# Kernel optimization log

Measured on AMD Instinct MI355X. Metric: run time of the kernel, lower is better.

Reference implementation:

```python
import jax, jax.numpy as jnp
import numpy as np

DECAY = 0.2
THRESH = 0.5
LENS = 0.5  # surrogate-gradient window half-width

@jax.custom_vjp
def spike(mem):
    # Heaviside spike at threshold (standard BP-SNN act_fun)
    return (mem > THRESH).astype(mem.dtype)

def _spike_fwd(mem):
    return spike(mem), mem

def _spike_bwd(mem, g):
    # rectangular surrogate gradient
    surr = (jnp.abs(mem - THRESH) < LENS).astype(mem.dtype)
    return (g * surr,)

spike.defvjp(_spike_fwd, _spike_bwd)


def setup_inputs() -> dict:
    key = jax.random.key(0)
    k1, k2, k3 = jax.random.split(key, 3)
    B, T, N_IN, N_H2, N_CLS = 2048, 50, 620, 620, 11
    x = jax.random.normal(k1, (B, T, N_IN), dtype=jnp.float32)
    # PyTorch Linear default init: U(-1/sqrt(fan_in), 1/sqrt(fan_in))
    b1 = 1.0 / np.sqrt(N_IN)
    b2 = 1.0 / np.sqrt(N_H2)
    W1 = jax.random.uniform(k2, (N_H2, N_IN), jnp.float32, -b1, b1)
    W2 = jax.random.uniform(k3, (N_CLS, N_H2), jnp.float32, -b2, b2)
    return {"x": x, "W1": W1, "W2": W2}


def reference(x, W1, W2):
    B = x.shape[0]
    T = x.shape[1]
    n_h2 = W1.shape[0]   # 620
    n_cls = W2.shape[0]  # 11

    def step(carry, xt):
        h1_mem, h1_spk, h2_mem, h2_spk, acc = carry
        # mem_update for layer 1: fc = Linear(no bias) + ReLU
        h1_mem = h1_mem * DECAY * (1.0 - h1_spk) + jax.nn.relu(xt @ W1.T)
        h1_spk = spike(h1_mem)
        # mem_update for layer 2
        h2_mem = h2_mem * DECAY * (1.0 - h2_spk) + jax.nn.relu(h1_spk @ W2.T)
        h2_spk = spike(h2_mem)
        return (h1_mem, h1_spk, h2_mem, h2_spk, acc + h2_spk), None

    z1 = jnp.zeros((B, n_h2), x.dtype)
    z2 = jnp.zeros((B, n_cls), x.dtype)
    carry0 = (z1, z1, z2, z2, z2)
    xs = jnp.swapaxes(x, 0, 1)  # [T, B, n_in]
    (_, _, _, _, sumspike), _ = jax.lax.scan(step, carry0, xs)
    return sumspike / 50.0
```

## Files before the change

kernel.cpp:

```cpp
#include <hip/hip_runtime.h>
#include <cstdint>
#include <cstddef>

#define B_TOT 2048
#define T_TOT 50
#define NIN   620
#define NH    620
#define NCLS  11

#define KC 384

#define BM 128
#define BN 128
#define KB 32

__global__ __launch_bounds__(256, 4)
void gemm_relu_kernel(const float* __restrict__ X,
                      const float* __restrict__ W1,
                      float* __restrict__ Z,
                      int t0, int ct)
{
    __shared__ float As[KB][BM + 4];
    __shared__ float Bs[KB][BN + 4];

    const int tid = threadIdx.x;
    const int n0 = blockIdx.x * BN;
    const int m0 = blockIdx.y * BM;
    const int tx = tid & 15;
    const int ty = tid >> 4;

    size_t a_off[4];
    size_t b_off[4];
    int    s_row[4], s_kl[4], b_ok[4];
#pragma unroll
    for (int it = 0; it < 4; ++it) {
        int task = tid + it * 256;
        int row  = (task >> 2) & 127;
        int kl   = (task >> 9) * 16 + (task & 3) * 4;
        s_row[it] = row;
        s_kl[it]  = kl;
        int m  = m0 + row;
        int bb = m / ct;
        int dt = m - bb * ct;
        a_off[it] = ((size_t)bb * T_TOT + (size_t)(t0 + dt)) * (size_t)NIN + kl;
        int n = n0 + row;
        b_off[it] = (size_t)n * NIN + kl;
        b_ok[it]  = (n < NH);
    }

    float acc[8][8];
#pragma unroll
    for (int i = 0; i < 8; ++i)
#pragma unroll
        for (int j = 0; j < 8; ++j) acc[i][j] = 0.0f;

    const int zc0 = n0 + tx * 4;
    const int zc1 = n0 + 64 + tx * 4;

    for (int k0 = 0; k0 < NIN; k0 += KB) {
#pragma unroll
        for (int it = 0; it < 4; ++it) {
            int k = k0 + s_kl[it];
            float4 av = make_float4(0.f, 0.f, 0.f, 0.f);
            if (k < NIN) av = *(const float4*)(X + a_off[it] + k0);
            As[s_kl[it] + 0][s_row[it]] = av.x;
            As[s_kl[it] + 1][s_row[it]] = av.y;
            As[s_kl[it] + 2][s_row[it]] = av.z;
            As[s_kl[it] + 3][s_row[it]] = av.w;
            float4 bv = make_float4(0.f, 0.f, 0.f, 0.f);
            if (b_ok[it] && k < NIN) bv = *(const float4*)(W1 + b_off[it] + k0);
            Bs[s_kl[it] + 0][s_row[it]] = bv.x;
            Bs[s_kl[it] + 1][s_row[it]] = bv.y;
            Bs[s_kl[it] + 2][s_row[it]] = bv.z;
            Bs[s_kl[it] + 3][s_row[it]] = bv.w;
        }
        __syncthreads();

#pragma unroll 8
        for (int kk = 0; kk < KB; ++kk) {
            float a[8], b[8];
            *(float4*)&a[0] = *(const float4*)&As[kk][ty * 8];
            *(float4*)&a[4] = *(const float4*)&As[kk][ty * 8 + 4];
            *(float4*)&b[0] = *(const float4*)&Bs[kk][tx * 4];
            *(float4*)&b[4] = *(const float4*)&Bs[kk][64 + tx * 4];
#pragma unroll
            for (int i = 0; i < 8; ++i)
#pragma unroll
                for (int j = 0; j < 8; ++j)
                    acc[i][j] = fmaf(a[i], b[j], acc[i][j]);
        }
        __syncthreads();

        if (k0 + KB == KC) {
#pragma unroll
            for (int i = 0; i < 8; ++i) {
                float* zr = Z + (size_t)(m0 + ty * 8 + i) * NH;
                if (zc0 < NH)
                    *(float4*)(zr + zc0) = make_float4(acc[i][0], acc[i][1],
                                                       acc[i][2], acc[i][3]);
                if (zc1 < NH)
                    *(float4*)(zr + zc1) = make_float4(acc[i][4], acc[i][5],
                                                       acc[i][6], acc[i][7]);
            }
#pragma unroll
            for (int i = 0; i < 8; ++i)
#pragma unroll
                for (int j = 0; j < 8; ++j) acc[i][j] = 0.0f;
        }
    }

#pragma unroll
    for (int i = 0; i < 8; ++i) {
        float* zr = Z + (size_t)(m0 + ty * 8 + i) * NH;
        if (zc0 < NH) {
            float4 p = *(const float4*)(zr + zc0);
            float4 v;
            v.x = fmaxf(__fadd_rn(p.x, acc[i][0]), 0.0f);
            v.y = fmaxf(__fadd_rn(p.y, acc[i][1]), 0.0f);
            v.z = fmaxf(__fadd_rn(p.z, acc[i][2]), 0.0f);
            v.w = fmaxf(__fadd_rn(p.w, acc[i][3]), 0.0f);
            *(float4*)(zr + zc0) = v;
        }
        if (zc1 < NH) {
            float4 p = *(const float4*)(zr + zc1);
            float4 v;
            v.x = fmaxf(__fadd_rn(p.x, acc[i][4]), 0.0f);
            v.y = fmaxf(__fadd_rn(p.y, acc[i][5]), 0.0f);
            v.z = fmaxf(__fadd_rn(p.z, acc[i][6]), 0.0f);
            v.w = fmaxf(__fadd_rn(p.w, acc[i][7]), 0.0f);
            *(float4*)(zr + zc1) = v;
        }
    }
}

#define NWAVE 4
__global__ __launch_bounds__(256)
void snn_kernel(const float* __restrict__ Z,
                const float* __restrict__ W2,
                float* __restrict__ state,
                float* __restrict__ out,
                int t0, int ct)
{
    __shared__ float W2s[NCLS][NH];
    __shared__ float Ss[NWAVE][NH];

    const int tid = threadIdx.x;
    for (int i = tid; i < NCLS * NH; i += 256)
        ((float*)W2s)[i] = W2[i];
    __syncthreads();

    const int lane = tid & 63;
    const int wv   = tid >> 6;
    const int b    = blockIdx.x * NWAVE + wv;

    float* st_h1m = state;
    float* st_h1s = state + (size_t)B_TOT * NH;
    float* st_h2m = state + (size_t)2 * B_TOT * NH;
    float* st_h2s = st_h2m + (size_t)B_TOT * NCLS;
    float* st_acc = st_h2s + (size_t)B_TOT * NCLS;

    float h1m[10], h1s[10];
    float h2m = 0.f, h2s = 0.f, acc = 0.f;

    if (t0 == 0) {
#pragma unroll
        for (int i = 0; i < 10; ++i) { h1m[i] = 0.f; h1s[i] = 0.f; }
    } else {
#pragma unroll
        for (int i = 0; i < 10; ++i) {
            int k = i * 64 + lane;
            if (k < NH) {
                h1m[i] = st_h1m[(size_t)b * NH + k];
                h1s[i] = st_h1s[(size_t)b * NH + k];
            } else { h1m[i] = 0.f; h1s[i] = 0.f; }
        }
        if (lane < NCLS) {
            h2m = st_h2m[(size_t)b * NCLS + lane];
            h2s = st_h2s[(size_t)b * NCLS + lane];
            acc = st_acc[(size_t)b * NCLS + lane];
        }
    }

    const int cls   = lane & 31;
    const int qbase = (lane < 32) ? 0 : (KC / 4);
    const int qcnt  = (lane < 32) ? (KC / 4) : ((NH - KC) / 4);

    for (int dt = 0; dt < ct; ++dt) {
        const float* z = Z + ((size_t)b * ct + dt) * NH;

#pragma unroll
        for (int i = 0; i < 10; ++i) {
            int k = i * 64 + lane;
            if (k < NH) {
                float dec = __fmul_rn(__fmul_rn(h1m[i], 0.2f), (1.0f - h1s[i]));
                float m = __fadd_rn(dec, z[k]);
                float s = (m > 0.5f) ? 1.0f : 0.0f;
                h1m[i] = m; h1s[i] = s;
                Ss[wv][k] = s;
            }
        }
        __syncthreads();

        float csum = 0.0f;
        if (cls < NCLS) {
            const float4* w4 = (const float4*)&W2s[cls][0] + qbase;
            const float4* s4 = (const float4*)&Ss[wv][0] + qbase;
            for (int q = 0; q < qcnt; ++q) {
                float4 w = w4[q];
                float4 s = s4[q];
                csum = fmaf(s.x, w.x, csum);
                csum = fmaf(s.y, w.y, csum);
                csum = fmaf(s.z, w.z, csum);
                csum = fmaf(s.w, w.w, csum);
            }
        }
        float csumB = __shfl_xor(csum, 32, 64);
        if (lane < NCLS) {
            float ctot = __fadd_rn(csum, csumB);
            float dec = __fmul_rn(__fmul_rn(h2m, 0.2f), (1.0f - h2s));
            float m = __fadd_rn(dec, fmaxf(ctot, 0.0f));
            float s = (m > 0.5f) ? 1.0f : 0.0f;
            h2m = m; h2s = s;
            acc = __fadd_rn(acc, s);
        }
        __syncthreads();
    }

    if (t0 + ct >= T_TOT) {
        if (lane < NCLS)
            out[(size_t)b * NCLS + lane] = __fdiv_rn(acc, 50.0f);
    } else {
#pragma unroll
        for (int i = 0; i < 10; ++i) {
            int k = i * 64 + lane;
            if (k < NH) {
                st_h1m[(size_t)b * NH + k] = h1m[i];
                st_h1s[(size_t)b * NH + k] = h1s[i];
            }
        }
        if (lane < NCLS) {
            st_h2m[(size_t)b * NCLS + lane] = h2m;
            st_h2s[(size_t)b * NCLS + lane] = h2s;
            st_acc[(size_t)b * NCLS + lane] = acc;
        }
    }
}

extern "C" void kernel_launch(void* const* d_in, const int* in_sizes, int n_in,
                              void* d_out, int out_size, void* d_ws, size_t ws_size,
                              hipStream_t stream)
{
    const float* X  = (const float*)d_in[0];
    const float* W1 = (const float*)d_in[1];
    const float* W2 = (const float*)d_in[2];
    float* out = (float*)d_out;

    const size_t state_floats = (size_t)2 * B_TOT * NH + (size_t)3 * B_TOT * NCLS;
    const size_t state_bytes  = state_floats * sizeof(float);
    const size_t bytes_per_t  = (size_t)B_TOT * NH * sizeof(float);

    size_t avail = (ws_size > state_bytes) ? (ws_size - state_bytes) : 0;
    int chunkT = (int)(avail / bytes_per_t);
    if (chunkT > T_TOT) chunkT = T_TOT;
    if (chunkT < 1) chunkT = 1;

    float* state = (float*)d_ws;
    float* Zbuf  = state + state_floats;

    for (int t0 = 0; t0 < T_TOT; t0 += chunkT) {
        int ct = (T_TOT - t0 < chunkT) ? (T_TOT - t0) : chunkT;
        dim3 ggrid((NH + BN - 1) / BN, (B_TOT * ct) / BM);
        gemm_relu_kernel<<<ggrid, 256, 0, stream>>>(X, W1, Zbuf, t0, ct);
        snn_kernel<<<dim3(B_TOT / NWAVE), 256, 0, stream>>>(Zbuf, W2, state, out, t0, ct);
    }
}
```

Before: 1.452 ms.

## Prefetch next GEMM K-tile into registers and batch LDS loads in readout dot

The layer-1 GEMM now loads the next K-tile of X and W1 into registers while the current tile is being multiplied, and stores it to shared memory after a barrier. This hides global-load latency behind the FMA loop at the cost of more registers. Separately, the layer-2 class dot-product loop is unrolled by 8, issuing batched shared-memory loads before the FMAs. The added register pressure may hurt occupancy under launch_bounds(256,4).

```diff
diff --git a/kernel.cpp b/kernel.cpp
--- a/kernel.cpp
+++ b/kernel.cpp
@@ -57,24 +57,45 @@
     const int zc0 = n0 + tx * 4;
     const int zc1 = n0 + 64 + tx * 4;
 
+    float4 pa[4], pb[4];
+
+#pragma unroll
+    for (int it = 0; it < 4; ++it) {
+        pa[it] = make_float4(0.f, 0.f, 0.f, 0.f);
+        pb[it] = make_float4(0.f, 0.f, 0.f, 0.f);
+        if (s_kl[it] < NIN) {
+            pa[it] = *(const float4*)(X + a_off[it]);
+            if (b_ok[it]) pb[it] = *(const float4*)(W1 + b_off[it]);
+        }
+    }
+#pragma unroll
+    for (int it = 0; it < 4; ++it) {
+        As[s_kl[it] + 0][s_row[it]] = pa[it].x;
+        As[s_kl[it] + 1][s_row[it]] = pa[it].y;
+        As[s_kl[it] + 2][s_row[it]] = pa[it].z;
+        As[s_kl[it] + 3][s_row[it]] = pa[it].w;
+        Bs[s_kl[it] + 0][s_row[it]] = pb[it].x;
+        Bs[s_kl[it] + 1][s_row[it]] = pb[it].y;
+        Bs[s_kl[it] + 2][s_row[it]] = pb[it].z;
+        Bs[s_kl[it] + 3][s_row[it]] = pb[it].w;
+    }
+
     for (int k0 = 0; k0 < NIN; k0 += KB) {
-#pragma unroll
-        for (int it = 0; it < 4; ++it) {
-            int k = k0 + s_kl[it];
-            float4 av = make_float4(0.f, 0.f, 0.f, 0.f);
-            if (k < NIN) av = *(const float4*)(X + a_off[it] + k0);
-            As[s_kl[it] + 0][s_row[it]] = av.x;
-            As[s_kl[it] + 1][s_row[it]] = av.y;
-            As[s_kl[it] + 2][s_row[it]] = av.z;
-            As[s_kl[it] + 3][s_row[it]] = av.w;
-            float4 bv = make_float4(0.f, 0.f, 0.f, 0.f);
-            if (b_ok[it] && k < NIN) bv = *(const float4*)(W1 + b_off[it] + k0);
-            Bs[s_kl[it] + 0][s_row[it]] = bv.x;
-            Bs[s_kl[it] + 1][s_row[it]] = bv.y;
-            Bs[s_kl[it] + 2][s_row[it]] = bv.z;
-            Bs[s_kl[it] + 3][s_row[it]] = bv.w;
-        }
         __syncthreads();
+
+        const int k0n = k0 + KB;
+        const bool has_next = (k0n < NIN);
+        if (has_next) {
+#pragma unroll
+            for (int it = 0; it < 4; ++it) {
+                pa[it] = make_float4(0.f, 0.f, 0.f, 0.f);
+                pb[it] = make_float4(0.f, 0.f, 0.f, 0.f);
+                if (k0n + s_kl[it] < NIN) {
+                    pa[it] = *(const float4*)(X + a_off[it] + k0n);
+                    if (b_ok[it]) pb[it] = *(const float4*)(W1 + b_off[it] + k0n);
+                }
+            }
+        }
 
 #pragma unroll 8
         for (int kk = 0; kk < KB; ++kk) {
@@ -89,7 +110,6 @@
                 for (int j = 0; j < 8; ++j)
                     acc[i][j] = fmaf(a[i], b[j], acc[i][j]);
         }
-        __syncthreads();
 
         if (k0 + KB == KC) {
 #pragma unroll
@@ -106,6 +126,22 @@
             for (int i = 0; i < 8; ++i)
 #pragma unroll
                 for (int j = 0; j < 8; ++j) acc[i][j] = 0.0f;
+        }
+
+        __syncthreads();
+
+        if (has_next) {
+#pragma unroll
+            for (int it = 0; it < 4; ++it) {
+                As[s_kl[it] + 0][s_row[it]] = pa[it].x;
+                As[s_kl[it] + 1][s_row[it]] = pa[it].y;
+                As[s_kl[it] + 2][s_row[it]] = pa[it].z;
+                As[s_kl[it] + 3][s_row[it]] = pa[it].w;
+                Bs[s_kl[it] + 0][s_row[it]] = pb[it].x;
+                Bs[s_kl[it] + 1][s_row[it]] = pb[it].y;
+                Bs[s_kl[it] + 2][s_row[it]] = pb[it].z;
+                Bs[s_kl[it] + 3][s_row[it]] = pb[it].w;
+            }
         }
     }
 
@@ -205,7 +241,20 @@
         if (cls < NCLS) {
             const float4* w4 = (const float4*)&W2s[cls][0] + qbase;
             const float4* s4 = (const float4*)&Ss[wv][0] + qbase;
-            for (int q = 0; q < qcnt; ++q) {
+            int q = 0;
+            for (; q + 8 <= qcnt; q += 8) {
+                float4 w[8], s[8];
+#pragma unroll
+                for (int u = 0; u < 8; ++u) { w[u] = w4[q + u]; s[u] = s4[q + u]; }
+#pragma unroll
+                for (int u = 0; u < 8; ++u) {
+                    csum = fmaf(s[u].x, w[u].x, csum);
+                    csum = fmaf(s[u].y, w[u].y, csum);
+                    csum = fmaf(s[u].z, w[u].z, csum);
+                    csum = fmaf(s[u].w, w[u].w, csum);
+                }
+            }
+            for (; q < qcnt; ++q) {
                 float4 w = w4[q];
                 float4 s = s4[q];
                 csum = fmaf(s.x, w.x, csum);
```

After: 1.606 ms. 1.11x slower.
